# Kernel optimization log

Measured on AMD Instinct MI355X. Metric: run time of the kernel, lower is better.

Reference implementation:

```python
import jax, jax.numpy as jnp
import numpy as np

K = 4096
N = 11008
GROUP_SIZE = 128
NUM_GROUPS = K // GROUP_SIZE
BATCH = 4
SEQ = 2048


def setup_inputs() -> dict:
    key = jax.random.key(0)
    kx, kw, ks = jax.random.split(key, 3)
    x = jax.random.normal(kx, (BATCH, SEQ, K), dtype=jnp.float16)
    # packed uint8 bytes, each holding two INT4 values (stored as int32)
    weight_packed = jax.random.randint(kw, (N, K // 2), 0, 256, dtype=jnp.int32)
    # positive group-wise scales ~ abs(randn)*0.1 -> uniform*0.1 is fine statistically
    scales = (jax.random.uniform(ks, (N, NUM_GROUPS), dtype=jnp.float32) * 0.1).astype(jnp.float16)
    return {"x": x, "weight_packed": weight_packed, "scales": scales}


def _dequantize(weight_packed, scales):
    # unpack: low nibble first, then high nibble -> (N, K) values in [0, 15]
    low = weight_packed & 15
    high = (weight_packed >> 4) & 15
    w_int = jnp.stack([low, high], axis=-1).reshape(weight_packed.shape[0], -1)  # (N, K)
    # symmetric dequant with implicit zero-point 8, group-wise scales
    scales_expanded = jnp.repeat(scales, GROUP_SIZE, axis=1)  # (N, K)
    return scales_expanded * (w_int.astype(jnp.float16) - jnp.float16(8.0))


def reference(x, weight_packed, scales):
    # Y = X @ W_dequant.T : (B, S, K) x (N, K) -> (B, S, N)
    w_dequant = _dequantize(weight_packed, scales)  # (N, K) fp16
    out = jnp.einsum('bsk,nk->bsn', x, w_dequant)
    return out.astype(jnp.float16)
```

## Files before the change

kernel.cpp:

```cpp
#include <hip/hip_runtime.h>
#include <stdint.h>


namespace {

typedef unsigned int u32;
typedef unsigned short u16;
typedef __attribute__((ext_vector_type(8))) short bf16x8;
typedef __attribute__((ext_vector_type(4))) float f32x4;
typedef __attribute__((ext_vector_type(4))) u32 u32x4;

constexpr int Mt = 8192;
constexpr int Nt = 11008;
constexpr int Kt = 4096;
constexpr int KP = Kt / 2;
constexpr int NG = 32;
constexpr int BM = 256;
constexpr int BN = 256;
constexpr int BK = 64;
constexpr int THREADS = 512;
constexpr int GRID = (Mt / BM) * (Nt / BN);
constexpr int NKT = Kt / BK;
constexpr int NB_CNT = Nt / BN;

__device__ __forceinline__ u16 f2bf(float f) {
  u32 u = __float_as_uint(f);
  return (u16)((u + 0x7FFFu + ((u >> 16) & 1u)) >> 16);
}
__device__ __forceinline__ u32 pk2bf(float a, float b) {
  return (u32)f2bf(a) | ((u32)f2bf(b) << 16);
}
__device__ __forceinline__ u32 dqpair(u32 b, float s, float c) {
  float f0 = (float)(b & 15u);
  float f1 = (float)((b >> 4) & 15u);
  return pk2bf(fmaf(f0, s, c), fmaf(f1, s, c));
}
__device__ __forceinline__ void async16(const void* g, void* l) {
  __builtin_amdgcn_global_load_lds(
      (const __attribute__((address_space(1))) u32*)g,
      (__attribute__((address_space(3))) u32*)l, 16, 0, 0);
}

__global__ __launch_bounds__(256) void cvt_x(const float* __restrict__ X,
                                             u32* __restrict__ O) {
  const int total = Mt * Kt / 4;
  for (int j = blockIdx.x * 256 + threadIdx.x; j < total;
       j += (int)(gridDim.x * 256)) {
    float4 v = ((const float4*)X)[j];
    ((uint2*)O)[j] = make_uint2(pk2bf(v.x, v.y), pk2bf(v.z, v.w));
  }
}

__global__ __launch_bounds__(256) void cvt_w(const int* __restrict__ W,
                                             const float* __restrict__ S,
                                             u32* __restrict__ O) {
  const int total = Nt * KP / 4;
  for (int j = blockIdx.x * 256 + threadIdx.x; j < total;
       j += (int)(gridDim.x * 256)) {
    int4 v = ((const int4*)W)[j];
    int vv[4] = {v.x, v.y, v.z, v.w};
    const int j0 = j * 4;
    const int row = j0 >> 11;
    const int jj = j0 & 2047;
    const float* sr = S + (size_t)row * NG;
    u32x4 o;
    #pragma unroll
    for (int e = 0; e < 4; ++e) {
      float s = sr[(jj + e) >> 6];
      o[e] = dqpair((u32)vv[e], s, -8.f * s);
    }
    ((u32x4*)O)[j] = o;
  }
}

__global__ __launch_bounds__(THREADS, 2) void gemm8p(
    const u16* __restrict__ Xb, const u16* __restrict__ Wb,
    float* __restrict__ Y) {
  __shared__ __align__(16) unsigned char smem[131072];

  const int tid  = (int)threadIdx.x;
  const int lane = tid & 63;
  const int wid  = tid >> 6;
  const int wm   = wid >> 2;
  const int wn   = wid & 3;

  const int bid = (int)blockIdx.x;
  const int wg  = (bid & 7) * (GRID / 8) + (bid >> 3);
  const int mb  = wg / NB_CNT;
  const int nb  = wg - mb * NB_CNT;
  const int m0  = mb * BM;
  const int n0  = nb * BN;

  const int srow = tid >> 3;
  const int sswz = (tid & 7) ^ (srow & 7);
  const u16* aRow = Xb + (size_t)(m0 + srow) * Kt + sswz * 8;
  const u16* bRow = Wb + (size_t)(n0 + (srow >> 5) * 64 + (srow & 31)) * Kt + sswz * 8;
  const int ldst = tid * 16;

  const int frow = lane & 15;
  const int fk   = lane >> 4;
  const int s0o  = ((fk ^ (lane & 7)) << 4);
  const int s1o  = (((4 + fk) ^ (lane & 7)) << 4);
  const int aRdC = (wm * 64 + frow) * 128;
  const int bRdC = (wn * 32 + frow) * 128;

  f32x4 acc[8][4];
  #pragma unroll
  for (int i = 0; i < 8; ++i)
    #pragma unroll
    for (int j = 0; j < 4; ++j) acc[i][j] = f32x4{0.f, 0.f, 0.f, 0.f};

  #define GATE(n) asm volatile("s_waitcnt vmcnt(" #n ")" ::: "memory")
  #define BARR()  asm volatile("s_barrier" ::: "memory")

  #define STAGE_A(g, buf, kt)                                                  \
    do {                                                                       \
      unsigned char* d_ = smem + (buf) * 32768 + (g) * 16384 + ldst;           \
      const u16* s_ = aRow + (size_t)((g) * 64) * Kt + (kt) * 64;              \
      async16(s_, d_);                                                         \
      async16(s_ + (size_t)128 * Kt, d_ + 8192);                               \
    } while (0)
  #define STAGE_B(p, buf, kt)                                                  \
    do {                                                                       \
      unsigned char* d_ = smem + 65536 + (buf) * 32768 + (p) * 16384 + ldst;   \
      const u16* s_ = bRow + (size_t)((p) * 32) * Kt + (kt) * 64;              \
      async16(s_, d_);                                                         \
      async16(s_ + (size_t)128 * Kt, d_ + 8192);                               \
    } while (0)

  #define LD_A(dst, g, buf)                                                    \
    do {                                                                       \
      const unsigned char* b_ = smem + (buf) * 32768 + (g) * 16384 + aRdC;     \
      _Pragma("unroll")                                                        \
      for (int q_ = 0; q_ < 4; ++q_) {                                         \
        dst[q_][0] = *(const bf16x8*)(b_ + q_ * 2048 + s0o);                   \
        dst[q_][1] = *(const bf16x8*)(b_ + q_ * 2048 + s1o);                   \
      }                                                                        \
    } while (0)
  #define LD_B(dst, p, buf)                                                    \
    do {                                                                       \
      const unsigned char* b_ =                                                \
          smem + 65536 + (buf) * 32768 + (p) * 16384 + bRdC;                   \
      _Pragma("unroll")                                                        \
      for (int q_ = 0; q_ < 2; ++q_) {                                         \
        dst[q_][0] = *(const bf16x8*)(b_ + q_ * 2048 + s0o);                   \
        dst[q_][1] = *(const bf16x8*)(b_ + q_ * 2048 + s1o);                   \
      }                                                                        \
    } while (0)

  #define MM_G(FG, FNP, A_, B_, GN)                                            \
    do {                                                                       \
      BARR();                                                                  \
      __builtin_amdgcn_s_setprio(1);                                           \
      _Pragma("unroll")                                                        \
      for (int fm_ = 0; fm_ < 4; ++fm_)                                        \
        _Pragma("unroll")                                                      \
        for (int fn_ = 0; fn_ < 2; ++fn_)                                      \
          _Pragma("unroll")                                                    \
          for (int kk_ = 0; kk_ < 2; ++kk_)                                    \
            acc[(FG) * 4 + fm_][(FNP) * 2 + fn_] =                             \
                __builtin_amdgcn_mfma_f32_16x16x32_bf16(                       \
                    A_[fm_][kk_], B_[fn_][kk_],                                \
                    acc[(FG) * 4 + fm_][(FNP) * 2 + fn_], 0, 0, 0);            \
      __builtin_amdgcn_s_setprio(0);                                           \
      if ((GN) == 6) { asm volatile("s_waitcnt vmcnt(6)" ::: "memory"); }      \
      else if ((GN) == 0) { asm volatile("s_waitcnt vmcnt(0)" ::: "memory"); } \
      BARR();                                                                  \
    } while (0)

  #define TILE(BUF, T, GN_LAST)                                                \
    do {                                                                       \
      LD_A(af, 0, BUF);                                                        \
      LD_B(b0, 0, BUF);                                                        \
      STAGE_A(1, BUF ^ 1, (T) + 1);                                            \
      MM_G(0, 0, af, b0, -1);                                                  \
      LD_B(b1, 1, BUF);                                                        \
      STAGE_A(0, BUF, (T) + 2);                                                \
      MM_G(0, 1, af, b1, -1);                                                  \
      LD_A(af, 1, BUF);                                                        \
      STAGE_B(0, BUF, (T) + 2);                                                \
      MM_G(1, 0, af, b0, -1);                                                  \
      STAGE_B(1, BUF, (T) + 2);                                                \
      MM_G(1, 1, af, b1, GN_LAST);                                             \
    } while (0)

  bf16x8 af[4][2], b0[2][2], b1[2][2];

  STAGE_A(0, 0, 0);
  STAGE_B(0, 0, 0);
  STAGE_B(1, 0, 0);
  STAGE_A(1, 0, 0);
  STAGE_A(0, 1, 1);
  STAGE_B(0, 1, 1);
  STAGE_B(1, 1, 1);
  GATE(6);
  BARR();

  #pragma unroll 1
  for (int t0 = 0; t0 < NKT - 2; t0 += 2) {
    TILE(0, t0, 6);
    TILE(1, t0 + 1, 6);
  }

  {
    LD_A(af, 0, 0);
    LD_B(b0, 0, 0);
    STAGE_A(1, 1, 63);
    MM_G(0, 0, af, b0, -1);
    LD_B(b1, 1, 0);
    MM_G(0, 1, af, b1, -1);
    LD_A(af, 1, 0);
    MM_G(1, 0, af, b0, -1);
    MM_G(1, 1, af, b1, 0);
  }
  {
    LD_A(af, 0, 1);
    LD_B(b0, 0, 1);
    MM_G(0, 0, af, b0, -1);
    LD_B(b1, 1, 1);
    MM_G(0, 1, af, b1, -1);
    LD_A(af, 1, 1);
    MM_G(1, 0, af, b0, -1);
    MM_G(1, 1, af, b1, -1);
  }

  #undef GATE
  #undef BARR
  #undef STAGE_A
  #undef STAGE_B
  #undef LD_A
  #undef LD_B
  #undef MM_G
  #undef TILE

  #pragma unroll
  for (int fm = 0; fm < 8; ++fm) {
    #pragma unroll
    for (int r = 0; r < 4; ++r) {
      const size_t mrow = (size_t)(m0 + wm * 128 + fm * 16 + fk * 4 + r) * Nt;
      #pragma unroll
      for (int fn = 0; fn < 4; ++fn) {
        Y[mrow + (size_t)(n0 + wn * 64 + fn * 16 + frow)] = acc[fm][fn][r];
      }
    }
  }
}

__global__ __launch_bounds__(512) void gemm_fused(
    const float* __restrict__ Xf, const int* __restrict__ W,
    const float* __restrict__ S, float* __restrict__ Y) {
  constexpr int FBN = 128;
  constexpr int FNB = Nt / FBN;
  constexpr int FBK = 64;
  constexpr int FNKT = Kt / FBK;
  __shared__ __align__(16) unsigned char Alds[BM * FBK * 2];
  __shared__ __align__(16) unsigned char Blds[FBN * FBK * 2];

  const int tid = (int)threadIdx.x;
  const int lane = tid & 63;
  const int wid = tid >> 6;
  const int wm = wid >> 1;
  const int wn = wid & 1;

  const int bid = (int)blockIdx.x;
  const int fgrid = (Mt / BM) * FNB;
  const int wg = (bid & 7) * (fgrid / 8) + (bid >> 3);
  const int mb = wg / FNB;
  const int nb = wg - mb * FNB;
  const int m0 = mb * BM;
  const int n0 = nb * FBN;

  const int frow = lane & 15;
  const int fk = lane >> 4;
  const int fswz = (lane & 7) << 4;
  const unsigned char* aRd = Alds + (wm * 64 + frow) * 128;
  const unsigned char* bRd = Blds + (wn * 64 + frow) * 128;

  f32x4 acc[4][4];
  #pragma unroll
  for (int i = 0; i < 4; ++i)
    #pragma unroll
    for (int j = 0; j < 4; ++j) acc[i][j] = f32x4{0.f, 0.f, 0.f, 0.f};

  const int arow = tid >> 3, acol = tid & 7;
  const float* fA = Xf + (size_t)(m0 + arow) * Kt + acol * 8;
  unsigned char* fAD = Alds + arow * 128 + ((acol ^ (arow & 7)) << 4);
  const int nloc = tid >> 3, c4 = tid & 7;
  const int* fB0 = W + (size_t)(n0 + nloc) * KP + c4 * 4;
  const int* fB1 = fB0 + (size_t)64 * KP;
  const float* sp0 = S + (size_t)(n0 + nloc) * NG;
  const float* sp1 = sp0 + (size_t)64 * NG;
  unsigned char* fBD0 = Blds + nloc * 128 + ((c4 ^ (nloc & 7)) << 4);
  unsigned char* fBD1 = fBD0 + 64 * 128;

  #pragma unroll 1
  for (int kt = 0; kt < FNKT; ++kt) {
    const int k0 = kt * FBK;
    #pragma unroll
    for (int p = 0; p < 4; ++p) {
      float4 x0 = *(const float4*)(fA + (size_t)p * 64 * Kt + k0);
      float4 x1 = *(const float4*)(fA + (size_t)p * 64 * Kt + k0 + 4);
      u32x4 q;
      q[0] = pk2bf(x0.x, x0.y); q[1] = pk2bf(x0.z, x0.w);
      q[2] = pk2bf(x1.x, x1.y); q[3] = pk2bf(x1.z, x1.w);
      *(u32x4*)(fAD + p * 64 * 128) = q;
    }
    const int g = k0 >> 7;
    const float s0 = sp0[g], s1 = sp1[g];
    const float c0 = -8.f * s0, c1 = -8.f * s1;
    const int4 w0 = *(const int4*)(fB0 + (k0 >> 1));
    const int4 w1 = *(const int4*)(fB1 + (k0 >> 1));
    u32x4 q0, q1;
    q0[0] = dqpair((u32)w0.x, s0, c0); q0[1] = dqpair((u32)w0.y, s0, c0);
    q0[2] = dqpair((u32)w0.z, s0, c0); q0[3] = dqpair((u32)w0.w, s0, c0);
    q1[0] = dqpair((u32)w1.x, s1, c1); q1[1] = dqpair((u32)w1.y, s1, c1);
    q1[2] = dqpair((u32)w1.z, s1, c1); q1[3] = dqpair((u32)w1.w, s1, c1);
    *(u32x4*)fBD0 = q0;
    *(u32x4*)fBD1 = q1;

    __syncthreads();

    #pragma unroll
    for (int kk = 0; kk < 2; ++kk) {
      const int koff = (kk * 64 + fk * 16) ^ fswz;
      bf16x8 af[4], bfr[4];
      #pragma unroll
      for (int fm = 0; fm < 4; ++fm)
        af[fm] = *(const bf16x8*)(aRd + fm * 16 * 128 + koff);
      #pragma unroll
      for (int fn = 0; fn < 4; ++fn)
        bfr[fn] = *(const bf16x8*)(bRd + fn * 16 * 128 + koff);
      #pragma unroll
      for (int fm = 0; fm < 4; ++fm)
        #pragma unroll
        for (int fn = 0; fn < 4; ++fn)
          acc[fm][fn] = __builtin_amdgcn_mfma_f32_16x16x32_bf16(
              af[fm], bfr[fn], acc[fm][fn], 0, 0, 0);
    }
    __syncthreads();
  }

  #pragma unroll
  for (int fm = 0; fm < 4; ++fm) {
    #pragma unroll
    for (int r = 0; r < 4; ++r) {
      const size_t mrow = (size_t)(m0 + wm * 64 + fm * 16 + fk * 4 + r) * Nt;
      #pragma unroll
      for (int fn = 0; fn < 4; ++fn)
        Y[mrow + (size_t)(n0 + wn * 64 + fn * 16 + frow)] = acc[fm][fn][r];
    }
  }
}

}

extern "C" void kernel_launch(void* const* d_in, const int* in_sizes, int n_in,
                              void* d_out, int out_size, void* d_ws, size_t ws_size,
                              hipStream_t stream) {
  (void)in_sizes; (void)n_in; (void)out_size;
  const float* X = (const float*)d_in[0];
  const int* W   = (const int*)d_in[1];
  const float* S = (const float*)d_in[2];
  float* Y       = (float*)d_out;

  const size_t xbytes = (size_t)Mt * Kt * 2;
  const size_t wbytes = (size_t)Nt * Kt * 2;

  if (ws_size >= xbytes + wbytes) {
    u16* Xb = (u16*)d_ws;
    u16* Wb = (u16*)((char*)d_ws + xbytes);
    cvt_x<<<dim3(2048), dim3(256), 0, stream>>>(X, (u32*)Xb);
    cvt_w<<<dim3(2048), dim3(256), 0, stream>>>(W, S, (u32*)Wb);
    gemm8p<<<dim3(GRID), dim3(THREADS), 0, stream>>>(Xb, Wb, Y);
  } else {
    gemm_fused<<<dim3((Mt / BM) * (Nt / 128)), dim3(512), 0, stream>>>(X, W, S, Y);
  }
}
```

Before: 704.6 us.

## Load B fragments directly from global to registers and 4-stage A in LDS

The GEMM no longer stages the weight (B) tile through shared memory. Each wave loads its B fragments straight from global memory into double-buffered registers one k-tile ahead. The freed LDS holds a 4-slot ring for the A tile, prefetched two tiles ahead, and there are fewer barriers per tile. This cuts LDS traffic and barrier count, but raises register pressure and relies on uncoalesced 16-byte global loads for B, which could hurt bandwidth or occupancy.

```diff
diff --git a/kernel.cpp b/kernel.cpp
--- a/kernel.cpp
+++ b/kernel.cpp
@@ -73,10 +73,10 @@
   }
 }
 
-__global__ __launch_bounds__(THREADS, 2) void gemm8p(
+__global__ __launch_bounds__(THREADS, 2) void gemmbr(
     const u16* __restrict__ Xb, const u16* __restrict__ Wb,
     float* __restrict__ Y) {
-  __shared__ __align__(16) unsigned char smem[131072];
+  __shared__ __align__(16) unsigned char smem[4 * 32768];
 
   const int tid  = (int)threadIdx.x;
   const int lane = tid & 63;
@@ -94,15 +94,14 @@
   const int srow = tid >> 3;
   const int sswz = (tid & 7) ^ (srow & 7);
   const u16* aRow = Xb + (size_t)(m0 + srow) * Kt + sswz * 8;
-  const u16* bRow = Wb + (size_t)(n0 + (srow >> 5) * 64 + (srow & 31)) * Kt + sswz * 8;
   const int ldst = tid * 16;
 
   const int frow = lane & 15;
   const int fk   = lane >> 4;
   const int s0o  = ((fk ^ (lane & 7)) << 4);
   const int s1o  = (((4 + fk) ^ (lane & 7)) << 4);
-  const int aRdC = (wm * 64 + frow) * 128;
-  const int bRdC = (wn * 32 + frow) * 128;
+
+  const u16* wB = Wb + (size_t)(n0 + wn * 64 + frow) * Kt + fk * 8;
 
   f32x4 acc[8][4];
   #pragma unroll
@@ -113,124 +112,106 @@
   #define GATE(n) asm volatile("s_waitcnt vmcnt(" #n ")" ::: "memory")
   #define BARR()  asm volatile("s_barrier" ::: "memory")
 
-  #define STAGE_A(g, buf, kt)                                                  \
-    do {                                                                       \
-      unsigned char* d_ = smem + (buf) * 32768 + (g) * 16384 + ldst;           \
-      const u16* s_ = aRow + (size_t)((g) * 64) * Kt + (kt) * 64;              \
+  #define STAGE_A(SLOT, KT)                                                    \
+    do {                                                                       \
+      unsigned char* d_ = smem + (SLOT) * 32768 + ldst;                        \
+      const u16* s_ = aRow + (KT) * 64;                                        \
       async16(s_, d_);                                                         \
-      async16(s_ + (size_t)128 * Kt, d_ + 8192);                               \
-    } while (0)
-  #define STAGE_B(p, buf, kt)                                                  \
-    do {                                                                       \
-      unsigned char* d_ = smem + 65536 + (buf) * 32768 + (p) * 16384 + ldst;   \
-      const u16* s_ = bRow + (size_t)((p) * 32) * Kt + (kt) * 64;              \
-      async16(s_, d_);                                                         \
-      async16(s_ + (size_t)128 * Kt, d_ + 8192);                               \
-    } while (0)
-
-  #define LD_A(dst, g, buf)                                                    \
-    do {                                                                       \
-      const unsigned char* b_ = smem + (buf) * 32768 + (g) * 16384 + aRdC;     \
+      async16(s_ + (size_t)64 * Kt, d_ + 8192);                                \
+      async16(s_ + (size_t)128 * Kt, d_ + 16384);                              \
+      async16(s_ + (size_t)192 * Kt, d_ + 24576);                              \
+    } while (0)
+
+  #define LD_A(FG, SLOT)                                                       \
+    do {                                                                       \
+      const unsigned char* b_ =                                                \
+          smem + (SLOT) * 32768 + (wm * 128 + (FG) * 64 + frow) * 128;         \
       _Pragma("unroll")                                                        \
       for (int q_ = 0; q_ < 4; ++q_) {                                         \
-        dst[q_][0] = *(const bf16x8*)(b_ + q_ * 2048 + s0o);                   \
-        dst[q_][1] = *(const bf16x8*)(b_ + q_ * 2048 + s1o);                   \
+        af[q_][0] = *(const bf16x8*)(b_ + q_ * 2048 + s0o);                    \
+        af[q_][1] = *(const bf16x8*)(b_ + q_ * 2048 + s1o);                    \
       }                                                                        \
     } while (0)
-  #define LD_B(dst, p, buf)                                                    \
-    do {                                                                       \
-      const unsigned char* b_ =                                                \
-          smem + 65536 + (buf) * 32768 + (p) * 16384 + bRdC;                   \
+
+  #define LOADB(DST, KT)                                                       \
+    do {                                                                       \
       _Pragma("unroll")                                                        \
-      for (int q_ = 0; q_ < 2; ++q_) {                                         \
-        dst[q_][0] = *(const bf16x8*)(b_ + q_ * 2048 + s0o);                   \
-        dst[q_][1] = *(const bf16x8*)(b_ + q_ * 2048 + s1o);                   \
+      for (int fn_ = 0; fn_ < 4; ++fn_) {                                      \
+        _Pragma("unroll")                                                      \
+        for (int kk_ = 0; kk_ < 2; ++kk_)                                      \
+          DST[fn_][kk_] = *(const bf16x8*)(wB + (size_t)fn_ * 16 * Kt +        \
+                                           (KT) * 64 + kk_ * 32);              \
       }                                                                        \
     } while (0)
 
-  #define MM_G(FG, FNP, A_, B_, GN)                                            \
-    do {                                                                       \
-      BARR();                                                                  \
+  #define MMQ(FG, FNP, BS)                                                     \
+    do {                                                                       \
       __builtin_amdgcn_s_setprio(1);                                           \
       _Pragma("unroll")                                                        \
-      for (int fm_ = 0; fm_ < 4; ++fm_)                                        \
+      for (int q_ = 0; q_ < 4; ++q_)                                           \
         _Pragma("unroll")                                                      \
         for (int fn_ = 0; fn_ < 2; ++fn_)                                      \
           _Pragma("unroll")                                                    \
           for (int kk_ = 0; kk_ < 2; ++kk_)                                    \
-            acc[(FG) * 4 + fm_][(FNP) * 2 + fn_] =                             \
+            acc[(FG) * 4 + q_][(FNP) * 2 + fn_] =                              \
                 __builtin_amdgcn_mfma_f32_16x16x32_bf16(                       \
-                    A_[fm_][kk_], B_[fn_][kk_],                                \
-                    acc[(FG) * 4 + fm_][(FNP) * 2 + fn_], 0, 0, 0);            \
+                    af[q_][kk_], BS[(FNP) * 2 + fn_][kk_],                     \
+                    acc[(FG) * 4 + q_][(FNP) * 2 + fn_], 0, 0, 0);             \
       __builtin_amdgcn_s_setprio(0);                                           \
-      if ((GN) == 6) { asm volatile("s_waitcnt vmcnt(6)" ::: "memory"); }      \
-      else if ((GN) == 0) { asm volatile("s_waitcnt vmcnt(0)" ::: "memory"); } \
+    } while (0)
+
+  #define TILE(SLOT, SSLOT, BC, BN_, T, GATESTMT, DOSTAGE, DOB)                \
+    do {                                                                       \
+      LD_A(0, SLOT);                                                           \
+      if (DOSTAGE) STAGE_A(SSLOT, (T) + 2);                                    \
+      if (DOB) LOADB(BN_, (T) + 1);                                            \
       BARR();                                                                  \
-    } while (0)
-
-  #define TILE(BUF, T, GN_LAST)                                                \
-    do {                                                                       \
-      LD_A(af, 0, BUF);                                                        \
-      LD_B(b0, 0, BUF);                                                        \
-      STAGE_A(1, BUF ^ 1, (T) + 1);                                            \
-      MM_G(0, 0, af, b0, -1);                                                  \
-      LD_B(b1, 1, BUF);                                                        \
-      STAGE_A(0, BUF, (T) + 2);                                                \
-      MM_G(0, 1, af, b1, -1);                                                  \
-      LD_A(af, 1, BUF);                                                        \
-      STAGE_B(0, BUF, (T) + 2);                                                \
-      MM_G(1, 0, af, b0, -1);                                                  \
-      STAGE_B(1, BUF, (T) + 2);                                                \
-      MM_G(1, 1, af, b1, GN_LAST);                                             \
-    } while (0)
-
-  bf16x8 af[4][2], b0[2][2], b1[2][2];
-
-  STAGE_A(0, 0, 0);
-  STAGE_B(0, 0, 0);
-  STAGE_B(1, 0, 0);
-  STAGE_A(1, 0, 0);
-  STAGE_A(0, 1, 1);
-  STAGE_B(0, 1, 1);
-  STAGE_B(1, 1, 1);
-  GATE(6);
+      MMQ(0, 0, BC);                                                           \
+      MMQ(0, 1, BC);                                                           \
+      __builtin_amdgcn_sched_barrier(0);                                       \
+      LD_A(1, SLOT);                                                           \
+      MMQ(1, 0, BC);                                                           \
+      MMQ(1, 1, BC);                                                           \
+      GATESTMT;                                                                \
+      BARR();                                                                  \
+    } while (0)
+
+  bf16x8 af[4][2];
+  bf16x8 bs0[4][2], bs1[4][2];
+
+  STAGE_A(0, 0);
+  STAGE_A(1, 1);
+  LOADB(bs0, 0);
+  GATE(12);
   BARR();
 
   #pragma unroll 1
-  for (int t0 = 0; t0 < NKT - 2; t0 += 2) {
-    TILE(0, t0, 6);
-    TILE(1, t0 + 1, 6);
-  }
-
+  for (int t0 = 0; t0 < 60; t0 += 4) {
+    TILE(0, 2, bs0, bs1, t0,     GATE(20), 1, 1);
+    TILE(1, 3, bs1, bs0, t0 + 1, GATE(20), 1, 1);
+    TILE(2, 0, bs0, bs1, t0 + 2, GATE(20), 1, 1);
+    TILE(3, 1, bs1, bs0, t0 + 3, GATE(20), 1, 1);
+  }
+  TILE(0, 2, bs0, bs1, 60, GATE(20), 1, 1);
+  TILE(1, 3, bs1, bs0, 61, GATE(20), 1, 1);
+  TILE(2, 0, bs0, bs1, 62, GATE(16), 0, 1);
   {
-    LD_A(af, 0, 0);
-    LD_B(b0, 0, 0);
-    STAGE_A(1, 1, 63);
-    MM_G(0, 0, af, b0, -1);
-    LD_B(b1, 1, 0);
-    MM_G(0, 1, af, b1, -1);
-    LD_A(af, 1, 0);
-    MM_G(1, 0, af, b0, -1);
-    MM_G(1, 1, af, b1, 0);
-  }
-  {
-    LD_A(af, 0, 1);
-    LD_B(b0, 0, 1);
-    MM_G(0, 0, af, b0, -1);
-    LD_B(b1, 1, 1);
-    MM_G(0, 1, af, b1, -1);
-    LD_A(af, 1, 1);
-    MM_G(1, 0, af, b0, -1);
-    MM_G(1, 1, af, b1, -1);
+    LD_A(0, 3);
+    BARR();
+    MMQ(0, 0, bs1);
+    MMQ(0, 1, bs1);
+    __builtin_amdgcn_sched_barrier(0);
+    LD_A(1, 3);
+    MMQ(1, 0, bs1);
+    MMQ(1, 1, bs1);
   }
 
   #undef GATE
   #undef BARR
   #undef STAGE_A
-  #undef STAGE_B
   #undef LD_A
-  #undef LD_B
-  #undef MM_G
+  #undef LOADB
+  #undef MMQ
   #undef TILE
 
   #pragma unroll
@@ -371,7 +352,7 @@
     u16* Wb = (u16*)((char*)d_ws + xbytes);
     cvt_x<<<dim3(2048), dim3(256), 0, stream>>>(X, (u32*)Xb);
     cvt_w<<<dim3(2048), dim3(256), 0, stream>>>(W, S, (u32*)Wb);
-    gemm8p<<<dim3(GRID), dim3(THREADS), 0, stream>>>(Xb, Wb, Y);
+    gemmbr<<<dim3(GRID), dim3(THREADS), 0, stream>>>(Xb, Wb, Y);
   } else {
     gemm_fused<<<dim3((Mt / BM) * (Nt / 128)), dim3(512), 0, stream>>>(X, W, S, Y);
   }
```

New measurement: 1.234 ms. +75.1%, slower.
